# Kernel optimization log

Hardware: AMD Instinct MI355X
Metric: run time of the kernel (lower is better)

## Reference

```python
import jax, jax.numpy as jnp
import numpy as np

BATCH = 32
N_LEVELS = (16384, 4096, 1024, 256)   # nodes at each mesh resolution
M_LEVELS = (4096, 1024, 256, 64)      # nodes after each Pool (downsample)
DEG = 6                               # directed edges per node
POOL_K = 3                            # nnz per row of downsample matrix
FILTERS = (3, 32, 32, 32, 64)         # channel chain of the 4 ChebConvs
K_CHEB = 6                            # Chebyshev polynomial order


def setup_inputs() -> dict:
    key = jax.random.key(0)
    ks = iter(jax.random.split(key, 64))
    inp = {"x": jax.random.normal(next(ks), (BATCH, N_LEVELS[0], FILTERS[0]), jnp.float32)}
    for i, N in enumerate(N_LEVELS):
        er = jnp.repeat(jnp.arange(N), DEG)
        off = jax.random.randint(next(ks), (N * DEG,), 1, N)
        inp[f"er{i}"] = er
        inp[f"ec{i}"] = (er + off) % N  # guaranteed no self loops
    for i, (M, N) in enumerate(zip(M_LEVELS, N_LEVELS)):
        inp[f"pr{i}"] = jnp.repeat(jnp.arange(M), POOL_K)
        inp[f"pc{i}"] = jax.random.randint(next(ks), (M * POOL_K,), 0, N)
        inp[f"pv{i}"] = jax.random.uniform(next(ks), (M * POOL_K,), jnp.float32)
    for i in range(4):
        fin, fout = FILTERS[i], FILTERS[i + 1]
        scale = 1.0 / np.sqrt(fin * K_CHEB)
        inp[f"W{i}"] = jax.random.normal(next(ks), (K_CHEB, fin, fout), jnp.float32) * scale
        inp[f"b{i}"] = jnp.zeros((fout,), jnp.float32)
    inp["enc_W"] = jax.random.normal(next(ks), (M_LEVELS[-1] * FILTERS[-1], 128), jnp.float32) * 0.1
    inp["enc_b"] = jnp.zeros((128,), jnp.float32)
    inp["cls_W"] = jax.random.normal(next(ks), (128, 10), jnp.float32) * 0.1
    inp["cls_b"] = jnp.zeros((10,), jnp.float32)
    return inp


def _cheb_conv(x, er, ec, W, b):
    # x: [B,N,Fin]; W: [K,Fin,Fout].
    # PyG ChebConv with lambda_max=2: L_hat = L - I = -D^{-1/2} A D^{-1/2}.
    N = x.shape[1]
    deg = jnp.zeros((N,), x.dtype).at[er].add(1.0)
    dinv = jnp.where(deg > 0, 1.0 / jnp.sqrt(jnp.maximum(deg, 1.0)), 0.0)
    norm = -(dinv[er] * dinv[ec])  # [E]

    def L(t):  # sparse matvec: gather neighbor feats, weight, scatter-add
        return jnp.zeros_like(t).at[:, er].add(t[:, ec] * norm[None, :, None])

    Tx0 = x
    out = jnp.einsum("bnf,fg->bng", Tx0, W[0])
    Tx1 = L(x)
    out = out + jnp.einsum("bnf,fg->bng", Tx1, W[1])
    for k in range(2, W.shape[0]):
        Tx2 = 2.0 * L(Tx1) - Tx0
        out = out + jnp.einsum("bnf,fg->bng", Tx2, W[k])
        Tx0, Tx1 = Tx1, Tx2
    return out + b


def _pool(x, pr, pc, pv, m):
    # sparse downsample matrix [m,N]: index_select cols * value, scatter_add rows
    B, _, F = x.shape
    return jnp.zeros((B, m, F), x.dtype).at[:, pr].add(x[:, pc] * pv[None, :, None])


def reference(x, er0, ec0, er1, ec1, er2, ec2, er3, ec3,
              pr0, pc0, pv0, pr1, pc1, pv1, pr2, pc2, pv2, pr3, pc3, pv3,
              W0, b0, W1, b1, W2, b2, W3, b3, enc_W, enc_b, cls_W, cls_b):
    ers, ecs = (er0, er1, er2, er3), (ec0, ec1, ec2, ec3)
    prs, pcs, pvs = (pr0, pr1, pr2, pr3), (pc0, pc1, pc2, pc3), (pv0, pv1, pv2, pv3)
    Ws, bs = (W0, W1, W2, W3), (b0, b1, b2, b3)
    for i in range(4):  # fixed n_layers loop (structurally distinct layers)
        x = jax.nn.relu(_cheb_conv(x, ers[i], ecs[i], Ws[i], bs[i]))
        x = _pool(x, prs[i], pcs[i], pvs[i], M_LEVELS[i])
    x = x.reshape(x.shape[0], -1)  # [B, 64*64]
    h = jax.nn.relu(x @ enc_W + enc_b)
    return h @ cls_W + cls_b
```

## Files before the change

kernel.cpp:

```cpp
#include <hip/hip_runtime.h>
#include <hip/hip_fp16.h>
#include <cstddef>
#include <cstdint>

#define BATCH 32


struct alignas(8) half4 { __half2 lo, hi; };

__device__ __forceinline__ void h4f(const half4 h, float f[4]) {
  float2 a = __half22float2(h.lo);
  float2 c = __half22float2(h.hi);
  f[0] = a.x; f[1] = a.y; f[2] = c.x; f[3] = c.y;
}
__device__ __forceinline__ void fma4(float4& a, float s, const float4& w) {
  a.x += s * w.x; a.y += s * w.y; a.z += s * w.z; a.w += s * w.w;
}
__device__ __forceinline__ float4 relu4(const float4& a) {
  return make_float4(fmaxf(a.x, 0.f), fmaxf(a.y, 0.f), fmaxf(a.z, 0.f), fmaxf(a.w, 0.f));
}

__global__ void __launch_bounds__(256) transpose_h(
    const float* __restrict__ x, half4* __restrict__ xh)
{
  int t = blockIdx.x * 256 + threadIdx.x;
  int n = t >> 5;
  int b = t & 31;
  const float* src = x + ((size_t)b * 16384 + n) * 3;
  half4 h;
  h.lo = __floats2half2_rn(src[0], src[1]);
  h.hi = __floats2half2_rn(src[2], 0.f);
  xh[t] = h;
}

template<int N>
__global__ void __launch_bounds__(256) cheb_step_h(
    const half4* __restrict__ Tin, const half4* __restrict__ Tpp,
    const int* __restrict__ ec, half4* __restrict__ Tout,
    float coef, float beta)
{
  int idx = blockIdx.x * 256 + threadIdx.x;
  int n = idx >> 5;
  int b = idx & 31;
  const int* e = ec + n * 6;
  float s0 = 0.f, s1 = 0.f, s2 = 0.f;
#pragma unroll
  for (int d = 0; d < 6; ++d) {
    half4 v = Tin[(e[d] << 5) | b];
    float2 a = __half22float2(v.lo);
    float2 c = __half22float2(v.hi);
    s0 += a.x; s1 += a.y; s2 += c.x;
  }
  half4 p = Tpp[idx];
  float2 pa = __half22float2(p.lo);
  float2 pc = __half22float2(p.hi);
  half4 o;
  o.lo = __floats2half2_rn(coef * s0 + beta * pa.x, coef * s1 + beta * pa.y);
  o.hi = __floats2half2_rn(coef * s2 + beta * pc.x, 0.f);
  Tout[idx] = o;
}

template<int N, int M, int FOUT>
__global__ void __launch_bounds__(256) pool_conv_f3_h(
    const half4* __restrict__ Xh, const half4* __restrict__ T,
    const float* __restrict__ W, const float* __restrict__ bias,
    const int* __restrict__ pc, const float* __restrict__ pv,
    float* __restrict__ out)
{
  constexpr int F4 = FOUT / 4;
  constexpr size_t SL = (size_t)N * 32;
  __shared__ float Ws[6 * 3 * FOUT];
  for (int i = threadIdx.x; i < 6 * 3 * FOUT; i += 256) Ws[i] = W[i];
  __syncthreads();
  const float4* Ws4 = (const float4*)Ws;
  int t = blockIdx.x * 256 + threadIdx.x;
  int fo4 = t % F4;
  int b   = (t / F4) % BATCH;
  int m   = t / (F4 * BATCH);
  int c0 = pc[m * 3 + 0], c1 = pc[m * 3 + 1], c2 = pc[m * 3 + 2];
  float v0 = pv[m * 3 + 0], v1 = pv[m * 3 + 1], v2 = pv[m * 3 + 2];
  float4 bi = ((const float4*)bias)[fo4];
  float4 a0 = bi, a1 = bi, a2 = bi;
#pragma unroll
  for (int k = 0; k < 6; ++k) {
    const half4* base = (k == 0) ? Xh : (T + (size_t)(k - 1) * SL);
    float r0[4], r1[4], r2[4];
    h4f(base[(c0 << 5) | b], r0);
    h4f(base[(c1 << 5) | b], r1);
    h4f(base[(c2 << 5) | b], r2);
#pragma unroll
    for (int f = 0; f < 3; ++f) {
      float4 w = Ws4[(k * 3 + f) * F4 + fo4];
      fma4(a0, r0[f], w);
      fma4(a1, r1[f], w);
      fma4(a2, r2[f], w);
    }
  }
  a0 = relu4(a0); a1 = relu4(a1); a2 = relu4(a2);
  float4 acc;
  acc.x = v0*a0.x + v1*a1.x + v2*a2.x;
  acc.y = v0*a0.y + v1*a1.y + v2*a2.y;
  acc.z = v0*a0.z + v1*a1.z + v2*a2.z;
  acc.w = v0*a0.w + v1*a1.w + v2*a2.w;
  ((float4*)out)[((size_t)m * BATCH + b) * F4 + fo4] = acc;
}

template<int N, int F, int THREADS, int MINW>
__global__ void __launch_bounds__(THREADS, MINW) cheb_recur_h4(
    const float* __restrict__ X,
    const int* __restrict__ ec,
    __half* __restrict__ Th)
{
  constexpr int NPT = N / THREADS;
  __shared__ float4 cur[N];
  const float cI = -1.0f / 6.0f;
  const float cS = -1.0f / 3.0f;
  const int b = blockIdx.x & 31;
  const int fbase = (blockIdx.x >> 5) * 4;
  constexpr size_t SLH = (size_t)N * 32 * F;
  float4 prevv[NPT];
#pragma unroll
  for (int i = 0; i < NPT; ++i) {
    int n = threadIdx.x + i * THREADS;
    cur[n] = *(const float4*)(X + ((size_t)n * 32 + b) * F + fbase);
  }
  __syncthreads();
#pragma unroll 1
  for (int k = 1; k <= 5; ++k) {
    float4 newv[NPT];
    __half* Tk = Th + (size_t)(k - 1) * SLH;
#pragma unroll
    for (int i = 0; i < NPT; ++i) {
      int n = threadIdx.x + i * THREADS;
      const int* e = ec + n * 6;
      float4 s = make_float4(0.f, 0.f, 0.f, 0.f);
#pragma unroll
      for (int d = 0; d < 6; ++d) {
        float4 t = cur[e[d]];
        s.x += t.x; s.y += t.y; s.z += t.z; s.w += t.w;
      }
      float4 v;
      if (k == 1) {
        v.x = cI * s.x; v.y = cI * s.y; v.z = cI * s.z; v.w = cI * s.w;
      } else {
        v.x = cS * s.x - prevv[i].x; v.y = cS * s.y - prevv[i].y;
        v.z = cS * s.z - prevv[i].z; v.w = cS * s.w - prevv[i].w;
      }
      newv[i] = v;
      half4 h;
      h.lo = __floats2half2_rn(v.x, v.y);
      h.hi = __floats2half2_rn(v.z, v.w);
      *(half4*)(Tk + ((size_t)n * 32 + b) * F + fbase) = h;
    }
    __syncthreads();
#pragma unroll
    for (int i = 0; i < NPT; ++i) {
      int n = threadIdx.x + i * THREADS;
      prevv[i] = cur[n];
      cur[n] = newv[i];
    }
    __syncthreads();
  }
}

template<int N, int M, int FOUT, bool OUT_BM>
__global__ void __launch_bounds__(256) pool_conv_v32_h(
    const float* __restrict__ X, const __half* __restrict__ Th,
    const float* __restrict__ W, const float* __restrict__ bias,
    const int* __restrict__ pc, const float* __restrict__ pv,
    float* __restrict__ out)
{
  constexpr int FIN = 32;
  constexpr int F4 = FOUT / 4;
  constexpr size_t SLH = (size_t)N * 32 * FIN;
  __shared__ float Ws[6 * FIN * FOUT];
  for (int i = threadIdx.x; i < 6 * FIN * FOUT; i += 256) Ws[i] = W[i];
  __syncthreads();
  const float4* Ws4 = (const float4*)Ws;
  const float4* X4p = (const float4*)X;
  int t = blockIdx.x * 256 + threadIdx.x;
  int fo4 = t % F4;
  int b   = (t / F4) % BATCH;
  int m   = t / (F4 * BATCH);
  int c0 = pc[m * 3 + 0], c1 = pc[m * 3 + 1], c2 = pc[m * 3 + 2];
  float v0 = pv[m * 3 + 0], v1 = pv[m * 3 + 1], v2 = pv[m * 3 + 2];
  float4 bi = ((const float4*)bias)[fo4];
  float4 a0 = bi, a1 = bi, a2 = bi;
  {
    const float4* r0 = X4p + ((size_t)c0 * BATCH + b) * 8;
    const float4* r1 = X4p + ((size_t)c1 * BATCH + b) * 8;
    const float4* r2 = X4p + ((size_t)c2 * BATCH + b) * 8;
#pragma unroll
    for (int fi = 0; fi < 8; ++fi) {
      float4 t0 = r0[fi], t1 = r1[fi], t2 = r2[fi];
#pragma unroll
      for (int ff = 0; ff < 4; ++ff) {
        float4 w = Ws4[(fi * 4 + ff) * F4 + fo4];
        fma4(a0, ((const float*)&t0)[ff], w);
        fma4(a1, ((const float*)&t1)[ff], w);
        fma4(a2, ((const float*)&t2)[ff], w);
      }
    }
  }
#pragma unroll 1
  for (int k = 1; k < 6; ++k) {
    const half4* base = (const half4*)(Th + (size_t)(k - 1) * SLH);
    const half4* r0 = base + ((size_t)c0 * 32 + b) * 8;
    const half4* r1 = base + ((size_t)c1 * 32 + b) * 8;
    const half4* r2 = base + ((size_t)c2 * 32 + b) * 8;
#pragma unroll
    for (int q = 0; q < 8; ++q) {
      float f0[4], f1[4], f2[4];
      h4f(r0[q], f0); h4f(r1[q], f1); h4f(r2[q], f2);
#pragma unroll
      for (int ff = 0; ff < 4; ++ff) {
        float4 w = Ws4[((k * 32) + q * 4 + ff) * F4 + fo4];
        fma4(a0, f0[ff], w);
        fma4(a1, f1[ff], w);
        fma4(a2, f2[ff], w);
      }
    }
  }
  a0 = relu4(a0); a1 = relu4(a1); a2 = relu4(a2);
  float4 acc;
  acc.x = v0*a0.x + v1*a1.x + v2*a2.x;
  acc.y = v0*a0.y + v1*a1.y + v2*a2.y;
  acc.z = v0*a0.z + v1*a1.z + v2*a2.z;
  acc.w = v0*a0.w + v1*a1.w + v2*a2.w;
  size_t oi = OUT_BM ? (((size_t)b * M + m) * F4 + fo4) : (((size_t)m * BATCH + b) * F4 + fo4);
  ((float4*)out)[oi] = acc;
}

__global__ void __launch_bounds__(256) encoder_partial(
    const float* __restrict__ Xf, const float* __restrict__ encW,
    float* __restrict__ partial)
{
  int b  = blockIdx.x;
  int ks = blockIdx.y;
  int fo = threadIdx.x & 127;
  int half = threadIdx.x >> 7;
  const float* xr = Xf + b * 4096 + ks * 256 + half * 128;
  const float* w  = encW + (size_t)(ks * 256 + half * 128) * 128;
  float acc = 0.f;
#pragma unroll 8
  for (int i = 0; i < 128; ++i) acc += xr[i] * w[(size_t)i * 128 + fo];
  __shared__ float part[256];
  part[threadIdx.x] = acc;
  __syncthreads();
  if (half == 0) partial[(size_t)(b * 16 + ks) * 128 + fo] = part[fo] + part[128 + fo];
}

__global__ void __launch_bounds__(128) encoder_reduce_cls(
    const float* __restrict__ partial, const float* __restrict__ encB,
    const float* __restrict__ clsW, const float* __restrict__ clsB,
    float* __restrict__ out)
{
  int b = blockIdx.x;
  int fo = threadIdx.x;
  float acc = encB[fo];
#pragma unroll
  for (int ks = 0; ks < 16; ++ks) acc += partial[(size_t)(b * 16 + ks) * 128 + fo];
  __shared__ float Hs[128];
  Hs[fo] = fmaxf(acc, 0.f);
  __syncthreads();
  if (fo < 10) {
    float s = clsB[fo];
#pragma unroll 4
    for (int f = 0; f < 128; ++f) s += Hs[f] * clsW[f * 10 + fo];
    out[b * 10 + fo] = s;
  }
}

extern "C" void kernel_launch(void* const* d_in, const int* in_sizes, int n_in,
                              void* d_out, int out_size, void* d_ws, size_t ws_size,
                              hipStream_t stream)
{
  const float* x   = (const float*)d_in[0];
  const int* ec0 = (const int*)d_in[2];
  const int* ec1 = (const int*)d_in[4];
  const int* ec2 = (const int*)d_in[6];
  const int* ec3 = (const int*)d_in[8];
  const int* pc0 = (const int*)d_in[10]; const float* pv0 = (const float*)d_in[11];
  const int* pc1 = (const int*)d_in[13]; const float* pv1 = (const float*)d_in[14];
  const int* pc2 = (const int*)d_in[16]; const float* pv2 = (const float*)d_in[17];
  const int* pc3 = (const int*)d_in[19]; const float* pv3 = (const float*)d_in[20];
  const float* W0 = (const float*)d_in[21]; const float* b0 = (const float*)d_in[22];
  const float* W1 = (const float*)d_in[23]; const float* b1 = (const float*)d_in[24];
  const float* W2 = (const float*)d_in[25]; const float* b2 = (const float*)d_in[26];
  const float* W3 = (const float*)d_in[27]; const float* b3 = (const float*)d_in[28];
  const float* encW = (const float*)d_in[29]; const float* encB = (const float*)d_in[30];
  const float* clsW = (const float*)d_in[31]; const float* clsB = (const float*)d_in[32];
  float* out = (float*)d_out;

  float* ws = (float*)d_ws;
  half4*  Xh = (half4*)ws;
  __half* Th = (__half*)(ws + 1048576);
  float* X1 = ws + 1048576 + 10485760;
  float* X2 = X1 + 4194304;
  float* X3 = X2 + 1048576;
  float* X4 = X3 + 262144;
  float* P  = X4 + 131072;

  const float cI = -1.0f / 6.0f;
  const float cS = -1.0f / 3.0f;
  dim3 blk(256);

  transpose_h<<<dim3(2048), blk, 0, stream>>>(x, Xh);

  {
    constexpr size_t S = (size_t)16384 * 32;
    half4* T4 = (half4*)Th;
    cheb_step_h<16384><<<dim3(2048), blk, 0, stream>>>(Xh,       Xh,       ec0, T4,        cI,  0.f);
    cheb_step_h<16384><<<dim3(2048), blk, 0, stream>>>(T4,       Xh,       ec0, T4 + S,    cS, -1.f);
    cheb_step_h<16384><<<dim3(2048), blk, 0, stream>>>(T4 + S,   T4,       ec0, T4 + 2*S,  cS, -1.f);
    cheb_step_h<16384><<<dim3(2048), blk, 0, stream>>>(T4 + 2*S, T4 + S,   ec0, T4 + 3*S,  cS, -1.f);
    cheb_step_h<16384><<<dim3(2048), blk, 0, stream>>>(T4 + 3*S, T4 + 2*S, ec0, T4 + 4*S,  cS, -1.f);
    pool_conv_f3_h<16384, 4096, 32><<<dim3(4096), blk, 0, stream>>>(
        Xh, (const half4*)Th, W0, b0, pc0, pv0, X1);
  }
  {
    cheb_recur_h4<4096, 32, 1024, 4><<<dim3(256), dim3(1024), 0, stream>>>(X1, ec1, Th);
    pool_conv_v32_h<4096, 1024, 32, false><<<dim3(1024), blk, 0, stream>>>(
        X1, Th, W1, b1, pc1, pv1, X2);
  }
  {
    cheb_recur_h4<1024, 32, 256, 4><<<dim3(256), blk, 0, stream>>>(X2, ec2, Th);
    pool_conv_v32_h<1024, 256, 32, false><<<dim3(256), blk, 0, stream>>>(
        X2, Th, W2, b2, pc2, pv2, X3);
  }
  {
    cheb_recur_h4<256, 32, 256, 4><<<dim3(256), blk, 0, stream>>>(X3, ec3, Th);
    pool_conv_v32_h<256, 64, 64, true><<<dim3(128), blk, 0, stream>>>(
        X3, Th, W3, b3, pc3, pv3, X4);
  }
  encoder_partial<<<dim3(32, 16), blk, 0, stream>>>(X4, encW, P);
  encoder_reduce_cls<<<dim3(32), dim3(128), 0, stream>>>(P, encB, clsW, clsB, out);
}
```

Baseline: 278.3 us.

## Fuse level-0 Chebyshev recurrence into one LDS-resident kernel per batch

Replaces the input transpose and five separate global-memory Chebyshev step kernels at the finest level with a single kernel. Each of its 32 blocks holds one batch's 16384-node signal in shared memory and runs all five recurrence steps there. The output layout becomes batch-major, and the level-0 pool/conv reads the raw input directly. The deeper-level recurrences now store their shared-memory state in half precision, which halves LDS traffic. The trade-off is that only 32 blocks run at level 0, leaving most of the GPU idle, and the half-precision state adds rounding error.

```diff
diff --git a/kernel.cpp b/kernel.cpp
--- a/kernel.cpp
+++ b/kernel.cpp
@@ -20,55 +20,81 @@
   return make_float4(fmaxf(a.x, 0.f), fmaxf(a.y, 0.f), fmaxf(a.z, 0.f), fmaxf(a.w, 0.f));
 }
 
-__global__ void __launch_bounds__(256) transpose_h(
-    const float* __restrict__ x, half4* __restrict__ xh)
-{
-  int t = blockIdx.x * 256 + threadIdx.x;
-  int n = t >> 5;
-  int b = t & 31;
-  const float* src = x + ((size_t)b * 16384 + n) * 3;
-  half4 h;
-  h.lo = __floats2half2_rn(src[0], src[1]);
-  h.hi = __floats2half2_rn(src[2], 0.f);
-  xh[t] = h;
-}
-
-template<int N>
-__global__ void __launch_bounds__(256) cheb_step_h(
-    const half4* __restrict__ Tin, const half4* __restrict__ Tpp,
-    const int* __restrict__ ec, half4* __restrict__ Tout,
-    float coef, float beta)
-{
-  int idx = blockIdx.x * 256 + threadIdx.x;
-  int n = idx >> 5;
-  int b = idx & 31;
-  const int* e = ec + n * 6;
-  float s0 = 0.f, s1 = 0.f, s2 = 0.f;
-#pragma unroll
-  for (int d = 0; d < 6; ++d) {
-    half4 v = Tin[(e[d] << 5) | b];
-    float2 a = __half22float2(v.lo);
-    float2 c = __half22float2(v.hi);
-    s0 += a.x; s1 += a.y; s2 += c.x;
-  }
-  half4 p = Tpp[idx];
-  float2 pa = __half22float2(p.lo);
-  float2 pc = __half22float2(p.hi);
-  half4 o;
-  o.lo = __floats2half2_rn(coef * s0 + beta * pa.x, coef * s1 + beta * pa.y);
-  o.hi = __floats2half2_rn(coef * s2 + beta * pc.x, 0.f);
-  Tout[idx] = o;
-}
-
-template<int N, int M, int FOUT>
-__global__ void __launch_bounds__(256) pool_conv_f3_h(
-    const half4* __restrict__ Xh, const half4* __restrict__ T,
+__global__ void __launch_bounds__(1024, 4) cheb_chain0(
+    const float* __restrict__ x,
+    const int* __restrict__ ec,
+    __half* __restrict__ Th)
+{
+  __shared__ half4 cur[16384];
+  const int b = blockIdx.x;
+  const float cI = -1.0f / 6.0f;
+  const float cS = -1.0f / 3.0f;
+  half4 prevv[16];
+  half4 newh[16];
+
+#pragma unroll
+  for (int i = 0; i < 16; ++i) {
+    int n = threadIdx.x + (i << 10);
+    const float* src = x + ((size_t)b * 16384 + n) * 3;
+    half4 h;
+    h.lo = __floats2half2_rn(src[0], src[1]);
+    h.hi = __floats2half2_rn(src[2], 0.f);
+    cur[n] = h;
+  }
+  __syncthreads();
+
+#pragma unroll 1
+  for (int k = 1; k <= 5; ++k) {
+    half4* Tk = (half4*)Th + (size_t)(k - 1) * 524288 + (size_t)b * 16384;
+#pragma unroll
+    for (int i = 0; i < 16; ++i) {
+      int n = threadIdx.x + (i << 10);
+      const int2* e2 = (const int2*)(ec + n * 6);
+      int2 ea = e2[0], eb = e2[1], ez = e2[2];
+      int na[6];
+      na[0] = ea.x; na[1] = ea.y; na[2] = eb.x;
+      na[3] = eb.y; na[4] = ez.x; na[5] = ez.y;
+      float s0 = 0.f, s1 = 0.f, s2 = 0.f;
+#pragma unroll
+      for (int d = 0; d < 6; ++d) {
+        half4 t = cur[na[d]];
+        float2 a = __half22float2(t.lo);
+        float2 c = __half22float2(t.hi);
+        s0 += a.x; s1 += a.y; s2 += c.x;
+      }
+      float v0, v1, v2;
+      if (k == 1) {
+        v0 = cI * s0; v1 = cI * s1; v2 = cI * s2;
+      } else {
+        float2 pa = __half22float2(prevv[i].lo);
+        float2 pc = __half22float2(prevv[i].hi);
+        v0 = cS * s0 - pa.x; v1 = cS * s1 - pa.y; v2 = cS * s2 - pc.x;
+      }
+      half4 h;
+      h.lo = __floats2half2_rn(v0, v1);
+      h.hi = __floats2half2_rn(v2, 0.f);
+      newh[i] = h;
+      Tk[n] = h;
+    }
+    __syncthreads();
+#pragma unroll
+    for (int i = 0; i < 16; ++i) {
+      int n = threadIdx.x + (i << 10);
+      prevv[i] = cur[n];
+      cur[n] = newh[i];
+    }
+    __syncthreads();
+  }
+}
+
+__global__ void __launch_bounds__(256) pool_conv_f3_bm(
+    const float* __restrict__ x, const half4* __restrict__ T,
     const float* __restrict__ W, const float* __restrict__ bias,
     const int* __restrict__ pc, const float* __restrict__ pv,
     float* __restrict__ out)
 {
+  constexpr int FOUT = 32;
   constexpr int F4 = FOUT / 4;
-  constexpr size_t SL = (size_t)N * 32;
   __shared__ float Ws[6 * 3 * FOUT];
   for (int i = threadIdx.x; i < 6 * 3 * FOUT; i += 256) Ws[i] = W[i];
   __syncthreads();
@@ -81,13 +107,25 @@
   float v0 = pv[m * 3 + 0], v1 = pv[m * 3 + 1], v2 = pv[m * 3 + 2];
   float4 bi = ((const float4*)bias)[fo4];
   float4 a0 = bi, a1 = bi, a2 = bi;
-#pragma unroll
-  for (int k = 0; k < 6; ++k) {
-    const half4* base = (k == 0) ? Xh : (T + (size_t)(k - 1) * SL);
+  {
+    const float* x0 = x + ((size_t)b * 16384 + c0) * 3;
+    const float* x1 = x + ((size_t)b * 16384 + c1) * 3;
+    const float* x2 = x + ((size_t)b * 16384 + c2) * 3;
+#pragma unroll
+    for (int f = 0; f < 3; ++f) {
+      float4 w = Ws4[f * F4 + fo4];
+      fma4(a0, x0[f], w);
+      fma4(a1, x1[f], w);
+      fma4(a2, x2[f], w);
+    }
+  }
+#pragma unroll
+  for (int k = 1; k < 6; ++k) {
+    const half4* base = T + (size_t)(k - 1) * 524288 + (size_t)b * 16384;
     float r0[4], r1[4], r2[4];
-    h4f(base[(c0 << 5) | b], r0);
-    h4f(base[(c1 << 5) | b], r1);
-    h4f(base[(c2 << 5) | b], r2);
+    h4f(base[c0], r0);
+    h4f(base[c1], r1);
+    h4f(base[c2], r2);
 #pragma unroll
     for (int f = 0; f < 3; ++f) {
       float4 w = Ws4[(k * 3 + f) * F4 + fo4];
@@ -106,50 +144,62 @@
 }
 
 template<int N, int F, int THREADS, int MINW>
-__global__ void __launch_bounds__(THREADS, MINW) cheb_recur_h4(
+__global__ void __launch_bounds__(THREADS, MINW) cheb_recur_hh(
     const float* __restrict__ X,
     const int* __restrict__ ec,
     __half* __restrict__ Th)
 {
   constexpr int NPT = N / THREADS;
-  __shared__ float4 cur[N];
+  __shared__ half4 cur[N];
   const float cI = -1.0f / 6.0f;
   const float cS = -1.0f / 3.0f;
   const int b = blockIdx.x & 31;
   const int fbase = (blockIdx.x >> 5) * 4;
   constexpr size_t SLH = (size_t)N * 32 * F;
-  float4 prevv[NPT];
+  half4 prevv[NPT];
+  half4 newh[NPT];
 #pragma unroll
   for (int i = 0; i < NPT; ++i) {
     int n = threadIdx.x + i * THREADS;
-    cur[n] = *(const float4*)(X + ((size_t)n * 32 + b) * F + fbase);
+    float4 xv = *(const float4*)(X + ((size_t)n * 32 + b) * F + fbase);
+    half4 h;
+    h.lo = __floats2half2_rn(xv.x, xv.y);
+    h.hi = __floats2half2_rn(xv.z, xv.w);
+    cur[n] = h;
   }
   __syncthreads();
 #pragma unroll 1
   for (int k = 1; k <= 5; ++k) {
-    float4 newv[NPT];
     __half* Tk = Th + (size_t)(k - 1) * SLH;
 #pragma unroll
     for (int i = 0; i < NPT; ++i) {
       int n = threadIdx.x + i * THREADS;
-      const int* e = ec + n * 6;
-      float4 s = make_float4(0.f, 0.f, 0.f, 0.f);
+      const int2* e2 = (const int2*)(ec + n * 6);
+      int2 ea = e2[0], eb = e2[1], ez = e2[2];
+      int na[6];
+      na[0] = ea.x; na[1] = ea.y; na[2] = eb.x;
+      na[3] = eb.y; na[4] = ez.x; na[5] = ez.y;
+      float s0 = 0.f, s1 = 0.f, s2 = 0.f, s3 = 0.f;
 #pragma unroll
       for (int d = 0; d < 6; ++d) {
-        float4 t = cur[e[d]];
-        s.x += t.x; s.y += t.y; s.z += t.z; s.w += t.w;
-      }
-      float4 v;
+        half4 t = cur[na[d]];
+        float2 a = __half22float2(t.lo);
+        float2 c = __half22float2(t.hi);
+        s0 += a.x; s1 += a.y; s2 += c.x; s3 += c.y;
+      }
+      float v0, v1, v2, v3;
       if (k == 1) {
-        v.x = cI * s.x; v.y = cI * s.y; v.z = cI * s.z; v.w = cI * s.w;
+        v0 = cI * s0; v1 = cI * s1; v2 = cI * s2; v3 = cI * s3;
       } else {
-        v.x = cS * s.x - prevv[i].x; v.y = cS * s.y - prevv[i].y;
-        v.z = cS * s.z - prevv[i].z; v.w = cS * s.w - prevv[i].w;
-      }
-      newv[i] = v;
+        float2 pa = __half22float2(prevv[i].lo);
+        float2 pc = __half22float2(prevv[i].hi);
+        v0 = cS * s0 - pa.x; v1 = cS * s1 - pa.y;
+        v2 = cS * s2 - pc.x; v3 = cS * s3 - pc.y;
+      }
       half4 h;
-      h.lo = __floats2half2_rn(v.x, v.y);
-      h.hi = __floats2half2_rn(v.z, v.w);
+      h.lo = __floats2half2_rn(v0, v1);
+      h.hi = __floats2half2_rn(v2, v3);
+      newh[i] = h;
       *(half4*)(Tk + ((size_t)n * 32 + b) * F + fbase) = h;
     }
     __syncthreads();
@@ -157,7 +207,7 @@
     for (int i = 0; i < NPT; ++i) {
       int n = threadIdx.x + i * THREADS;
       prevv[i] = cur[n];
-      cur[n] = newv[i];
+      cur[n] = newh[i];
     }
     __syncthreads();
   }
@@ -293,46 +343,31 @@
   float* out = (float*)d_out;
 
   float* ws = (float*)d_ws;
-  half4*  Xh = (half4*)ws;
-  __half* Th = (__half*)(ws + 1048576);
-  float* X1 = ws + 1048576 + 10485760;
+  __half* Th = (__half*)ws;
+  float* X1 = ws + 10485760;
   float* X2 = X1 + 4194304;
   float* X3 = X2 + 1048576;
   float* X4 = X3 + 262144;
   float* P  = X4 + 131072;
 
-  const float cI = -1.0f / 6.0f;
-  const float cS = -1.0f / 3.0f;
   dim3 blk(256);
 
-  transpose_h<<<dim3(2048), blk, 0, stream>>>(x, Xh);
-
-  {
-    constexpr size_t S = (size_t)16384 * 32;
-    half4* T4 = (half4*)Th;
-    cheb_step_h<16384><<<dim3(2048), blk, 0, stream>>>(Xh,       Xh,       ec0, T4,        cI,  0.f);
-    cheb_step_h<16384><<<dim3(2048), blk, 0, stream>>>(T4,       Xh,       ec0, T4 + S,    cS, -1.f);
-    cheb_step_h<16384><<<dim3(2048), blk, 0, stream>>>(T4 + S,   T4,       ec0, T4 + 2*S,  cS, -1.f);
-    cheb_step_h<16384><<<dim3(2048), blk, 0, stream>>>(T4 + 2*S, T4 + S,   ec0, T4 + 3*S,  cS, -1.f);
-    cheb_step_h<16384><<<dim3(2048), blk, 0, stream>>>(T4 + 3*S, T4 + 2*S, ec0, T4 + 4*S,  cS, -1.f);
-    pool_conv_f3_h<16384, 4096, 32><<<dim3(4096), blk, 0, stream>>>(
-        Xh, (const half4*)Th, W0, b0, pc0, pv0, X1);
-  }
-  {
-    cheb_recur_h4<4096, 32, 1024, 4><<<dim3(256), dim3(1024), 0, stream>>>(X1, ec1, Th);
-    pool_conv_v32_h<4096, 1024, 32, false><<<dim3(1024), blk, 0, stream>>>(
-        X1, Th, W1, b1, pc1, pv1, X2);
-  }
-  {
-    cheb_recur_h4<1024, 32, 256, 4><<<dim3(256), blk, 0, stream>>>(X2, ec2, Th);
-    pool_conv_v32_h<1024, 256, 32, false><<<dim3(256), blk, 0, stream>>>(
-        X2, Th, W2, b2, pc2, pv2, X3);
-  }
-  {
-    cheb_recur_h4<256, 32, 256, 4><<<dim3(256), blk, 0, stream>>>(X3, ec3, Th);
-    pool_conv_v32_h<256, 64, 64, true><<<dim3(128), blk, 0, stream>>>(
-        X3, Th, W3, b3, pc3, pv3, X4);
-  }
+  cheb_chain0<<<dim3(32), dim3(1024), 0, stream>>>(x, ec0, Th);
+  pool_conv_f3_bm<<<dim3(4096), blk, 0, stream>>>(
+      x, (const half4*)Th, W0, b0, pc0, pv0, X1);
+
+  cheb_recur_hh<4096, 32, 1024, 4><<<dim3(256), dim3(1024), 0, stream>>>(X1, ec1, Th);
+  pool_conv_v32_h<4096, 1024, 32, false><<<dim3(1024), blk, 0, stream>>>(
+      X1, Th, W1, b1, pc1, pv1, X2);
+
+  cheb_recur_hh<1024, 32, 256, 4><<<dim3(256), blk, 0, stream>>>(X2, ec2, Th);
+  pool_conv_v32_h<1024, 256, 32, false><<<dim3(256), blk, 0, stream>>>(
+      X2, Th, W2, b2, pc2, pv2, X3);
+
+  cheb_recur_hh<256, 32, 256, 4><<<dim3(256), blk, 0, stream>>>(X3, ec3, Th);
+  pool_conv_v32_h<256, 64, 64, true><<<dim3(128), blk, 0, stream>>>(
+      X3, Th, W3, b3, pc3, pv3, X4);
+
   encoder_partial<<<dim3(32, 16), blk, 0, stream>>>(X4, encW, P);
   encoder_reduce_cls<<<dim3(32), dim3(128), 0, stream>>>(P, encB, clsW, clsB, out);
 }
```

New measurement: 346.4 us. +24.5%, slower.

## Split level-0 half4 activations into batch-group-major layout for gather locality

Applied to the files above, without the earlier changes.

Level-0 half activations move from [node][32 batch] to [batch-group of 4][node][4]. Blocks are mapped so each one covers a single batch group over 64 nodes, and the neighbour gathers index only within that group. Each gathered node then touches 32 bytes instead of 256. The goal is to shrink the per-block working set so each batch group's slice stays in cache during the random gathers, at the cost of smaller contiguous chunks per gathered node. The edge indices are also loaded as int2 pairs.

```diff
diff --git a/kernel.cpp b/kernel.cpp
--- a/kernel.cpp
+++ b/kernel.cpp
@@ -20,37 +20,45 @@
   return make_float4(fmaxf(a.x, 0.f), fmaxf(a.y, 0.f), fmaxf(a.z, 0.f), fmaxf(a.w, 0.f));
 }
 
-__global__ void __launch_bounds__(256) transpose_h(
-    const float* __restrict__ x, half4* __restrict__ xh)
-{
-  int t = blockIdx.x * 256 + threadIdx.x;
-  int n = t >> 5;
-  int b = t & 31;
+__global__ void __launch_bounds__(256) transpose_b(
+    const float* __restrict__ x, half4* __restrict__ xb)
+{
+  int bg = blockIdx.x & 7;
+  int q  = blockIdx.x >> 3;
+  int b4 = threadIdx.x & 3;
+  int n  = q * 64 + (threadIdx.x >> 2);
+  int b  = bg * 4 + b4;
   const float* src = x + ((size_t)b * 16384 + n) * 3;
   half4 h;
   h.lo = __floats2half2_rn(src[0], src[1]);
   h.hi = __floats2half2_rn(src[2], 0.f);
-  xh[t] = h;
-}
-
-template<int N>
-__global__ void __launch_bounds__(256) cheb_step_h(
+  xb[((size_t)(bg << 14) + n) * 4 + b4] = h;
+}
+
+__global__ void __launch_bounds__(256) cheb_step_b(
     const half4* __restrict__ Tin, const half4* __restrict__ Tpp,
     const int* __restrict__ ec, half4* __restrict__ Tout,
     float coef, float beta)
 {
-  int idx = blockIdx.x * 256 + threadIdx.x;
-  int n = idx >> 5;
-  int b = idx & 31;
-  const int* e = ec + n * 6;
+  int bg = blockIdx.x & 7;
+  int q  = blockIdx.x >> 3;
+  int b4 = threadIdx.x & 3;
+  int n  = q * 64 + (threadIdx.x >> 2);
+  const half4* Tb = Tin + ((size_t)bg << 16);
+  const int2* e2 = (const int2*)(ec + n * 6);
+  int2 ea = e2[0], eb = e2[1], ez = e2[2];
+  int na[6];
+  na[0] = ea.x; na[1] = ea.y; na[2] = eb.x;
+  na[3] = eb.y; na[4] = ez.x; na[5] = ez.y;
   float s0 = 0.f, s1 = 0.f, s2 = 0.f;
 #pragma unroll
   for (int d = 0; d < 6; ++d) {
-    half4 v = Tin[(e[d] << 5) | b];
+    half4 v = Tb[(na[d] << 2) | b4];
     float2 a = __half22float2(v.lo);
     float2 c = __half22float2(v.hi);
     s0 += a.x; s1 += a.y; s2 += c.x;
   }
+  size_t idx = ((size_t)(bg << 14) + n) * 4 + b4;
   half4 p = Tpp[idx];
   float2 pa = __half22float2(p.lo);
   float2 pc = __half22float2(p.hi);
@@ -60,34 +68,36 @@
   Tout[idx] = o;
 }
 
-template<int N, int M, int FOUT>
-__global__ void __launch_bounds__(256) pool_conv_f3_h(
-    const half4* __restrict__ Xh, const half4* __restrict__ T,
+__global__ void __launch_bounds__(256) pool_conv_f3_b(
+    const half4* __restrict__ Xb, const half4* __restrict__ T,
     const float* __restrict__ W, const float* __restrict__ bias,
     const int* __restrict__ pc, const float* __restrict__ pv,
     float* __restrict__ out)
 {
-  constexpr int F4 = FOUT / 4;
-  constexpr size_t SL = (size_t)N * 32;
-  __shared__ float Ws[6 * 3 * FOUT];
-  for (int i = threadIdx.x; i < 6 * 3 * FOUT; i += 256) Ws[i] = W[i];
+  constexpr int F4 = 8;
+  constexpr size_t SL = (size_t)16384 * 32;
+  __shared__ float Ws[6 * 3 * 32];
+  for (int i = threadIdx.x; i < 6 * 3 * 32; i += 256) Ws[i] = W[i];
   __syncthreads();
   const float4* Ws4 = (const float4*)Ws;
-  int t = blockIdx.x * 256 + threadIdx.x;
-  int fo4 = t % F4;
-  int b   = (t / F4) % BATCH;
-  int m   = t / (F4 * BATCH);
+  int bg = blockIdx.x & 7;
+  int q  = blockIdx.x >> 3;
+  int fo4 = threadIdx.x & 7;
+  int b4  = (threadIdx.x >> 3) & 3;
+  int m   = q * 8 + (threadIdx.x >> 5);
+  int b   = bg * 4 + b4;
+  const size_t bgo = (size_t)bg << 16;
   int c0 = pc[m * 3 + 0], c1 = pc[m * 3 + 1], c2 = pc[m * 3 + 2];
   float v0 = pv[m * 3 + 0], v1 = pv[m * 3 + 1], v2 = pv[m * 3 + 2];
   float4 bi = ((const float4*)bias)[fo4];
   float4 a0 = bi, a1 = bi, a2 = bi;
 #pragma unroll
   for (int k = 0; k < 6; ++k) {
-    const half4* base = (k == 0) ? Xh : (T + (size_t)(k - 1) * SL);
+    const half4* base = ((k == 0) ? Xb : (T + (size_t)(k - 1) * SL)) + bgo;
     float r0[4], r1[4], r2[4];
-    h4f(base[(c0 << 5) | b], r0);
-    h4f(base[(c1 << 5) | b], r1);
-    h4f(base[(c2 << 5) | b], r2);
+    h4f(base[(c0 << 2) | b4], r0);
+    h4f(base[(c1 << 2) | b4], r1);
+    h4f(base[(c2 << 2) | b4], r2);
 #pragma unroll
     for (int f = 0; f < 3; ++f) {
       float4 w = Ws4[(k * 3 + f) * F4 + fo4];
@@ -293,7 +303,7 @@
   float* out = (float*)d_out;
 
   float* ws = (float*)d_ws;
-  half4*  Xh = (half4*)ws;
+  half4*  Xb = (half4*)ws;
   __half* Th = (__half*)(ws + 1048576);
   float* X1 = ws + 1048576 + 10485760;
   float* X2 = X1 + 4194304;
@@ -305,34 +315,31 @@
   const float cS = -1.0f / 3.0f;
   dim3 blk(256);
 
-  transpose_h<<<dim3(2048), blk, 0, stream>>>(x, Xh);
+  transpose_b<<<dim3(2048), blk, 0, stream>>>(x, Xb);
 
   {
     constexpr size_t S = (size_t)16384 * 32;
     half4* T4 = (half4*)Th;
-    cheb_step_h<16384><<<dim3(2048), blk, 0, stream>>>(Xh,       Xh,       ec0, T4,        cI,  0.f);
-    cheb_step_h<16384><<<dim3(2048), blk, 0, stream>>>(T4,       Xh,       ec0, T4 + S,    cS, -1.f);
-    cheb_step_h<16384><<<dim3(2048), blk, 0, stream>>>(T4 + S,   T4,       ec0, T4 + 2*S,  cS, -1.f);
-    cheb_step_h<16384><<<dim3(2048), blk, 0, stream>>>(T4 + 2*S, T4 + S,   ec0, T4 + 3*S,  cS, -1.f);
-    cheb_step_h<16384><<<dim3(2048), blk, 0, stream>>>(T4 + 3*S, T4 + 2*S, ec0, T4 + 4*S,  cS, -1.f);
-    pool_conv_f3_h<16384, 4096, 32><<<dim3(4096), blk, 0, stream>>>(
-        Xh, (const half4*)Th, W0, b0, pc0, pv0, X1);
-  }
-  {
-    cheb_recur_h4<4096, 32, 1024, 4><<<dim3(256), dim3(1024), 0, stream>>>(X1, ec1, Th);
-    pool_conv_v32_h<4096, 1024, 32, false><<<dim3(1024), blk, 0, stream>>>(
-        X1, Th, W1, b1, pc1, pv1, X2);
-  }
-  {
-    cheb_recur_h4<1024, 32, 256, 4><<<dim3(256), blk, 0, stream>>>(X2, ec2, Th);
-    pool_conv_v32_h<1024, 256, 32, false><<<dim3(256), blk, 0, stream>>>(
-        X2, Th, W2, b2, pc2, pv2, X3);
-  }
-  {
-    cheb_recur_h4<256, 32, 256, 4><<<dim3(256), blk, 0, stream>>>(X3, ec3, Th);
-    pool_conv_v32_h<256, 64, 64, true><<<dim3(128), blk, 0, stream>>>(
-        X3, Th, W3, b3, pc3, pv3, X4);
-  }
+    cheb_step_b<<<dim3(2048), blk, 0, stream>>>(Xb,       Xb,       ec0, T4,        cI,  0.f);
+    cheb_step_b<<<dim3(2048), blk, 0, stream>>>(T4,       Xb,       ec0, T4 + S,    cS, -1.f);
+    cheb_step_b<<<dim3(2048), blk, 0, stream>>>(T4 + S,   T4,       ec0, T4 + 2*S,  cS, -1.f);
+    cheb_step_b<<<dim3(2048), blk, 0, stream>>>(T4 + 2*S, T4 + S,   ec0, T4 + 3*S,  cS, -1.f);
+    cheb_step_b<<<dim3(2048), blk, 0, stream>>>(T4 + 3*S, T4 + 2*S, ec0, T4 + 4*S,  cS, -1.f);
+    pool_conv_f3_b<<<dim3(4096), blk, 0, stream>>>(
+        Xb, (const half4*)Th, W0, b0, pc0, pv0, X1);
+  }
+  cheb_recur_h4<4096, 32, 1024, 4><<<dim3(256), dim3(1024), 0, stream>>>(X1, ec1, Th);
+  pool_conv_v32_h<4096, 1024, 32, false><<<dim3(1024), blk, 0, stream>>>(
+      X1, Th, W1, b1, pc1, pv1, X2);
+
+  cheb_recur_h4<1024, 32, 256, 4><<<dim3(256), blk, 0, stream>>>(X2, ec2, Th);
+  pool_conv_v32_h<1024, 256, 32, false><<<dim3(256), blk, 0, stream>>>(
+      X2, Th, W2, b2, pc2, pv2, X3);
+
+  cheb_recur_h4<256, 32, 256, 4><<<dim3(256), blk, 0, stream>>>(X3, ec3, Th);
+  pool_conv_v32_h<256, 64, 64, true><<<dim3(128), blk, 0, stream>>>(
+      X3, Th, W3, b3, pc3, pv3, X4);
+
   encoder_partial<<<dim3(32, 16), blk, 0, stream>>>(X4, encW, P);
   encoder_reduce_cls<<<dim3(32), dim3(128), 0, stream>>>(P, encB, clsW, clsB, out);
 }
```

After: 283.5 us. No clear change (+1.9%).
